# Optimization experiments

Measured on AMD Instinct MI355X. Metric: run time of the kernel, lower is better.

## Reference

```python
import jax, jax.numpy as jnp
import numpy as np

NUM_HEADS = 8


def _conv3x3(x, w, b):
    # x: (B, C, H, W); w: (O, I, 3, 3) -> (B, O, H, W), stride 1, SAME padding
    y = jax.lax.conv_general_dilated(
        x, w, window_strides=(1, 1), padding='SAME',
        dimension_numbers=('NCHW', 'OIHW', 'NCHW'))
    return y + b[None, :, None, None]


def setup_inputs() -> dict:
    key = jax.random.key(0)
    ks = jax.random.split(key, 7)
    bs, mc, C, H, W = 2, 5, 640, 32, 32
    s = 0.02  # init scale for weights
    return {
        'x': jax.random.normal(ks[0], (bs, mc, C, H, W), jnp.float32),
        'wq': jax.random.normal(ks[1], (C, C, 3, 3), jnp.float32) * s,
        'bq': jnp.zeros((C,), jnp.float32),
        'wk': jax.random.normal(ks[2], (C, C, 3, 3), jnp.float32) * s,
        'bk': jnp.zeros((C,), jnp.float32),
        'wv': jax.random.normal(ks[3], (C, C, 3, 3), jnp.float32) * s,
        'bv': jnp.zeros((C,), jnp.float32),
        'w_proj': jax.random.normal(ks[4], (C, C), jnp.float32) * s,
        'b_proj': jnp.zeros((C,), jnp.float32),
    }


def reference(x, wq, bq, wk, bk, wv, bv, w_proj, b_proj):
    bs, mc, C, H, W = x.shape
    N = H * W
    nh = NUM_HEADS
    hd = C // nh
    scale = hd ** -0.5

    xf = x.reshape(bs * mc, C, H, W)

    def proj(w, b):
        # conv -> (bs, mc, nh, hd, N) -> (bs, mc, nh, N, hd)
        y = _conv3x3(xf, w, b).reshape(bs, mc, nh, hd, N)
        return y.transpose(0, 1, 2, 4, 3)

    q = proj(wq, bq)
    k = proj(wk, bk)
    v = proj(wv, bv)

    attn = jax.nn.softmax(jnp.einsum('bmhnd,bmhkd->bmhnk', q, k) * scale, axis=-1)
    o = jnp.einsum('bmhnk,bmhkd->bmhnd', attn, v)  # (bs, mc, nh, N, hd)

    # permute(0,3,1,2,4).reshape(bs, N, mc*C) then split back to (bs, N, mc, C)
    o = o.transpose(0, 3, 1, 2, 4).reshape(bs, N, mc, C)
    o = jnp.einsum('bnmc,dc->bnmd', o, w_proj) + b_proj  # Linear(C, C)
    return o.reshape(bs, N, mc * C)
```

## Files before the change

### kernel.cpp

```cpp
#include <hip/hip_runtime.h>

typedef _Float16 half_t;
typedef _Float16 half8 __attribute__((ext_vector_type(8)));
typedef _Float16 half4 __attribute__((ext_vector_type(4)));
typedef float floatx4 __attribute__((ext_vector_type(4)));
typedef unsigned int u32;

#define MFMA32(a,b,c) __builtin_amdgcn_mfma_f32_16x16x32_f16(a,b,c,0,0,0)
#define MFMA16(a,b,c) __builtin_amdgcn_mfma_f32_16x16x16f16(a,b,c,0,0,0)

#define XPAD_ELEMS (10u*34*34*640)
#define WR_ELEMS   (3u*9*640*640)
#define WP_ELEMS   (640u*640)
#define QKV_ELEMS  (10u*8*1024*80)
#define O_ELEMS    (10u*1024*640)

__device__ __forceinline__ void load16_lds(half_t* lds, const half_t* g) {
  __builtin_amdgcn_global_load_lds((const __attribute__((address_space(1))) u32*)g,
                                   (__attribute__((address_space(3))) u32*)lds,
                                   16, 0, 0);
}

__global__ __launch_bounds__(256) void k_convert_x(const float* __restrict__ x,
                                                   half_t* __restrict__ xpad) {
  const int img = blockIdx.x >> 5, y = blockIdx.x & 31;
  const float* src = x + (size_t)img*640*1024 + y*32;
  half_t* dst = xpad + (size_t)img*34*34*640;
  for (int i = threadIdx.x; i < 640*32; i += 256) {
    int xx = i / 640, c = i - xx*640;
    float v = src[(size_t)c*1024 + xx];
    dst[((size_t)(y+1)*34 + xx + 1)*640 + c] = (half_t)v;
  }
}

__global__ __launch_bounds__(256) void k_convert_w(const float* __restrict__ wq,
                                                   const float* __restrict__ wk,
                                                   const float* __restrict__ wv,
                                                   const float* __restrict__ wp,
                                                   half_t* __restrict__ wr2,
                                                   half_t* __restrict__ wp16) {
  const int p = blockIdx.y, row = blockIdx.x;
  if (p < 3) {
    const float* W = (p == 0) ? wq : (p == 1) ? wk : wv;
    for (int i = threadIdx.x; i < 5760; i += 256) {
      int t = i / 640, ci = i - t*640;
      wr2[(((size_t)p*640 + row)*9 + t)*640 + ci] = (half_t)W[((size_t)row*640 + ci)*9 + t];
    }
  } else {
    for (int i = threadIdx.x; i < 640; i += 256)
      wp16[(size_t)row*640 + i] = (half_t)wp[(size_t)row*640 + i];
  }
}

__global__ __launch_bounds__(256) void k_conv(const half_t* __restrict__ xpad,
                                              const half_t* __restrict__ wr2,
                                              const float* __restrict__ bq,
                                              const float* __restrict__ bk,
                                              const float* __restrict__ bv,
                                              half_t* __restrict__ qo,
                                              half_t* __restrict__ ko,
                                              half_t* __restrict__ vo) {
  __shared__ __align__(16) half_t sX[2][816*8];
  __shared__ __align__(16) half_t sW[4][512*8];
  const int tid = threadIdx.x;
  const int lane = tid & 63, wv = tid >> 6;
  const int l15 = lane & 15, lq = lane >> 4, lq16 = lq*16;
  const int mt = blockIdx.x, nt = blockIdx.y;
  const int proj = blockIdx.z / 10, img = blockIdx.z - proj*10;

  const half_t* xg = xpad + ((size_t)img*34*34 + (size_t)mt*4*34)*640;
  const half_t* wg = wr2 + ((size_t)proj*640 + nt*128)*5760;

  int xsrc[4], wsrc[2];
#pragma unroll
  for (int kk = 0; kk < 4; ++kk) {
    int idx = kk*256 + tid;
    int row = idx >> 2, slot = idx & 3;
    int chunk = slot ^ ((row >> 1) & 3);
    xsrc[kk] = row*640 + chunk*8;
  }
#pragma unroll
  for (int kk = 0; kk < 2; ++kk) {
    int idx = kk*256 + tid;
    int row = idx >> 2, slot = idx & 3;
    int chunk = slot ^ ((row >> 1) & 3);
    wsrc[kk] = row*5760 + chunk*8;
  }

  const int wrow = (wv >> 1)*64, wcol = (wv & 1)*64;
  int arow0[4];
#pragma unroll
  for (int fr = 0; fr < 4; ++fr) {
    int p = wrow + fr*16 + l15;
    arow0[fr] = (p >> 5)*34 + (p & 31);
  }
  int bboff[4];
#pragma unroll
  for (int fc = 0; fc < 4; ++fc) {
    int r = wcol + fc*16 + l15;
    bboff[fc] = (r << 6) + (lq16 ^ (((r >> 1) & 3) << 4));
  }

#pragma unroll
  for (int kk = 0; kk < 4; ++kk)
    if (kk < 3 || tid < 48)
      load16_lds(sX[0] + (size_t)(kk*256 + wv*64)*8, xg + xsrc[kk]);
#pragma unroll
  for (int kk = 0; kk < 2; ++kk)
    load16_lds(sW[0] + (size_t)(kk*256 + wv*64)*8, wg + wsrc[kk]);
#pragma unroll
  for (int kk = 0; kk < 2; ++kk)
    load16_lds(sW[1] + (size_t)(kk*256 + wv*64)*8, wg + wsrc[kk] + 640);

  floatx4 acc[4][4] = {};

  for (int g = 0; g < 20; ++g) {
#pragma unroll
    for (int t = 0; t < 9; ++t) {
      if (!(g == 19 && t >= 7)) {
        const int t2 = (t + 2 < 9) ? t + 2 : t - 7;
        const int g2 = (t + 2 < 9) ? g : g + 1;
        const int k0 = t2*640 + g2*32;
        half_t* wd = sW[(g + t + 2) & 3];
#pragma unroll
        for (int kk = 0; kk < 2; ++kk)
          load16_lds(wd + (size_t)(kk*256 + wv*64)*8, wg + wsrc[kk] + k0);
      }
      if (t == 7 && g < 19) {
        half_t* xd = sX[(g + 1) & 1];
#pragma unroll
        for (int kk = 0; kk < 4; ++kk)
          if (kk < 3 || tid < 48)
            load16_lds(xd + (size_t)(kk*256 + wv*64)*8, xg + xsrc[kk] + (g + 1)*32);
      }
      if (g == 19 && t == 7)      asm volatile("s_waitcnt vmcnt(2)" ::: "memory");
      else if (g == 19 && t == 8) asm volatile("s_waitcnt vmcnt(0)" ::: "memory");
      else if (t >= 7)            asm volatile("s_waitcnt vmcnt(8)" ::: "memory");
      else                        asm volatile("s_waitcnt vmcnt(4)" ::: "memory");
      __builtin_amdgcn_s_barrier();
      __builtin_amdgcn_sched_barrier(0);
      const char* sXc = (const char*)sX[g & 1];
      const char* sWc = (const char*)sW[(g + t) & 3];
      const int TR = (t/3)*34 + (t - (t/3)*3);
      half8 av[4], bw[4];
#pragma unroll
      for (int fr = 0; fr < 4; ++fr) {
        int r = arow0[fr] + TR;
        av[fr] = *(const half8*)(sXc + (r << 6) + (lq16 ^ (((r >> 1) & 3) << 4)));
      }
#pragma unroll
      for (int fc = 0; fc < 4; ++fc) bw[fc] = *(const half8*)(sWc + bboff[fc]);
      __builtin_amdgcn_s_setprio(1);
#pragma unroll
      for (int fr = 0; fr < 4; ++fr)
#pragma unroll
        for (int fc = 0; fc < 4; ++fc)
          acc[fr][fc] = MFMA32(av[fr], bw[fc], acc[fr][fc]);
      __builtin_amdgcn_s_setprio(0);
    }
  }

  const float* bias = (proj == 0) ? bq : (proj == 1) ? bk : bv;
#pragma unroll
  for (int fc = 0; fc < 4; ++fc) {
    int co = nt*128 + wcol + fc*16 + l15;
    float bb = bias[co];
    int hh = co / 80;
    int d = co - hh*80;
#pragma unroll
    for (int fr = 0; fr < 4; ++fr)
#pragma unroll
      for (int j = 0; j < 4; ++j) {
        int n = mt*128 + wrow + fr*16 + lq*4 + j;
        float val = acc[fr][fc][j] + bb;
        if (proj == 0)      qo[((size_t)(img*8 + hh)*1024 + n)*80 + d] = (half_t)(val * 0.11180339887498949f);
        else if (proj == 1) ko[((size_t)(img*8 + hh)*1024 + n)*80 + d] = (half_t)val;
        else                vo[((size_t)(img*8 + hh)*80 + d)*1024 + n] = (half_t)val;
      }
  }
}

__global__ __launch_bounds__(256) void k_attn(const half_t* __restrict__ qg_,
                                              const half_t* __restrict__ kg_,
                                              const half_t* __restrict__ vg_,
                                              half_t* __restrict__ og_) {
  __shared__ __align__(16) half_t sQ[128*80];
  __shared__ __align__(16) half_t sK[64*80];
  __shared__ __align__(16) half_t sV[80*64];
  __shared__ __align__(16) half_t sP[128*64];
  const int tid = threadIdx.x, lane = tid & 63, wv = tid >> 6;
  const int l15 = lane & 15, lq = lane >> 4;
  const int qt = blockIdx.x, gh = blockIdx.y;
  const half_t* qg = qg_ + ((size_t)gh*1024 + qt*128)*80;
  const half_t* kg = kg_ + (size_t)gh*1024*80;
  const half_t* vg = vg_ + (size_t)gh*80*1024;

#pragma unroll
  for (int kk = 0; kk < 5; ++kk)
    load16_lds(sQ + (size_t)(kk*256 + wv*64)*8, qg + (size_t)(kk*256 + tid)*8);

  float mrow[2][4], lrow[2][4];
  floatx4 oacc[2][5] = {};
#pragma unroll
  for (int fr = 0; fr < 2; ++fr)
#pragma unroll
    for (int j = 0; j < 4; ++j) { mrow[fr][j] = -1e30f; lrow[fr][j] = 0.f; }

  for (int kt = 0; kt < 16; ++kt) {
    __syncthreads();
#pragma unroll
    for (int kk = 0; kk < 3; ++kk) {
      int c = kk*256 + tid;
      if (c < 640) {
        int row = c / 10, cw = c - row*10;
        load16_lds(sK + (size_t)(kk*256 + wv*64)*8,
                   kg + ((size_t)kt*64 + row)*80 + cw*8);
      }
    }
#pragma unroll
    for (int kk = 0; kk < 3; ++kk) {
      int c = kk*256 + tid;
      if (c < 640) {
        load16_lds(sV + (size_t)(kk*256 + wv*64)*8,
                   vg + (size_t)(c >> 3)*1024 + kt*64 + (c & 7)*8);
      }
    }
    __syncthreads();

    const char* sQb = (const char*)sQ;
    const char* sKb = (const char*)sK;
    half8 qa0[2], qa1[2]; half4 qa2[2];
#pragma unroll
    for (int fr = 0; fr < 2; ++fr) {
      int r = wv*32 + fr*16 + l15;
      qa0[fr] = *(const half8*)(sQb + r*160 + lq*16);
      qa1[fr] = *(const half8*)(sQb + r*160 + 64 + lq*16);
      qa2[fr] = *(const half4*)(sQb + r*160 + 128 + lq*8);
    }
    floatx4 s[2][4];
#pragma unroll
    for (int fc = 0; fc < 4; ++fc) {
      int key = fc*16 + l15;
      half8 kb0 = *(const half8*)(sKb + key*160 + lq*16);
      half8 kb1 = *(const half8*)(sKb + key*160 + 64 + lq*16);
      half4 kb2 = *(const half4*)(sKb + key*160 + 128 + lq*8);
#pragma unroll
      for (int fr = 0; fr < 2; ++fr) {
        floatx4 t = {0.f, 0.f, 0.f, 0.f};
        t = MFMA16(qa2[fr], kb2, t);
        t = MFMA32(qa0[fr], kb0, t);
        t = MFMA32(qa1[fr], kb1, t);
        s[fr][fc] = t;
      }
    }

    float corr[2][4], psum[2][4];
#pragma unroll
    for (int fr = 0; fr < 2; ++fr)
#pragma unroll
      for (int j = 0; j < 4; ++j) {
        float mx = fmaxf(fmaxf(s[fr][0][j], s[fr][1][j]), fmaxf(s[fr][2][j], s[fr][3][j]));
        mx = fmaxf(mx, __shfl_xor(mx, 1));
        mx = fmaxf(mx, __shfl_xor(mx, 2));
        mx = fmaxf(mx, __shfl_xor(mx, 4));
        mx = fmaxf(mx, __shfl_xor(mx, 8));
        float mn = fmaxf(mrow[fr][j], mx);
        corr[fr][j] = __expf(mrow[fr][j] - mn);
        mrow[fr][j] = mn;
        psum[fr][j] = 0.f;
      }
#pragma unroll
    for (int fc = 0; fc < 4; ++fc)
#pragma unroll
      for (int fr = 0; fr < 2; ++fr)
#pragma unroll
        for (int j = 0; j < 4; ++j) {
          float p = __expf(s[fr][fc][j] - mrow[fr][j]);
          psum[fr][j] += p;
          sP[(size_t)(wv*32 + fr*16 + lq*4 + j)*64 + fc*16 + l15] = (half_t)p;
        }
#pragma unroll
    for (int fr = 0; fr < 2; ++fr)
#pragma unroll
      for (int j = 0; j < 4; ++j) {
        float t2 = psum[fr][j];
        t2 += __shfl_xor(t2, 1);
        t2 += __shfl_xor(t2, 2);
        t2 += __shfl_xor(t2, 4);
        t2 += __shfl_xor(t2, 8);
        lrow[fr][j] = lrow[fr][j]*corr[fr][j] + t2;
      }
#pragma unroll
    for (int fr = 0; fr < 2; ++fr)
#pragma unroll
      for (int fc = 0; fc < 5; ++fc)
#pragma unroll
        for (int j = 0; j < 4; ++j)
          oacc[fr][fc][j] *= corr[fr][j];

    __syncthreads();

    const char* sPb = (const char*)sP;
    const char* sVb = (const char*)sV;
    half8 pa[2][2];
#pragma unroll
    for (int fr = 0; fr < 2; ++fr) {
      int r = wv*32 + fr*16 + l15;
#pragma unroll
      for (int ks = 0; ks < 2; ++ks)
        pa[fr][ks] = *(const half8*)(sPb + r*128 + ks*64 + lq*16);
    }
#pragma unroll
    for (int fc = 0; fc < 5; ++fc)
#pragma unroll
      for (int ks = 0; ks < 2; ++ks) {
        half8 vb = *(const half8*)(sVb + (fc*16 + l15)*128 + ks*64 + lq*16);
#pragma unroll
        for (int fr = 0; fr < 2; ++fr)
          oacc[fr][fc] = MFMA32(pa[fr][ks], vb, oacc[fr][fc]);
      }
  }

  const int img = gh >> 3, hh = gh & 7;
  half_t* og = og_ + ((size_t)img*1024 + qt*128)*640 + hh*80;
#pragma unroll
  for (int fr = 0; fr < 2; ++fr)
#pragma unroll
    for (int j = 0; j < 4; ++j) {
      int n = wv*32 + fr*16 + lq*4 + j;
      float inv = 1.f / lrow[fr][j];
#pragma unroll
      for (int fc = 0; fc < 5; ++fc)
        og[(size_t)n*640 + fc*16 + l15] = (half_t)(oacc[fr][fc][j] * inv);
    }
}

__global__ __launch_bounds__(256) void k_proj(const half_t* __restrict__ oa,
                                              const half_t* __restrict__ wp,
                                              const float* __restrict__ bp,
                                              float* __restrict__ out) {
  __shared__ __align__(16) half_t sA[128*32];
  __shared__ __align__(16) half_t sB[128*32];
  const int tid = threadIdx.x, lane = tid & 63, wv = tid >> 6;
  const int l15 = lane & 15, lq = lane >> 4;
  const int mt = blockIdx.x, nt = blockIdx.y, img = blockIdx.z;
  const int bb = img / 5, mm = img - bb*5;
  const half_t* ag = oa + ((size_t)img*1024 + mt*128)*640;
  const half_t* bg = wp + (size_t)nt*128*640;
  const int wrow = (wv >> 1)*64, wcol = (wv & 1)*64;
  floatx4 acc[4][4] = {};
  for (int g = 0; g < 20; ++g) {
    __syncthreads();
#pragma unroll
    for (int kk = 0; kk < 2; ++kk) {
      int c = kk*256 + tid;
      load16_lds(sA + (size_t)(kk*256 + wv*64)*8, ag + (size_t)(c >> 2)*640 + g*32 + (c & 3)*8);
      load16_lds(sB + (size_t)(kk*256 + wv*64)*8, bg + (size_t)(c >> 2)*640 + g*32 + (c & 3)*8);
    }
    __syncthreads();
    const char* sAb = (const char*)sA;
    const char* sBb = (const char*)sB;
    half8 av[4], bw[4];
#pragma unroll
    for (int fr = 0; fr < 4; ++fr) av[fr] = *(const half8*)(sAb + (wrow + fr*16 + l15)*64 + lq*16);
#pragma unroll
    for (int fc = 0; fc < 4; ++fc) bw[fc] = *(const half8*)(sBb + (wcol + fc*16 + l15)*64 + lq*16);
#pragma unroll
    for (int fr = 0; fr < 4; ++fr)
#pragma unroll
      for (int fc = 0; fc < 4; ++fc)
        acc[fr][fc] = MFMA32(av[fr], bw[fc], acc[fr][fc]);
  }
  float* og = out + ((size_t)bb*1024 + mt*128)*3200 + mm*640 + nt*128;
#pragma unroll
  for (int fc = 0; fc < 4; ++fc) {
    float bias = bp[nt*128 + wcol + fc*16 + l15];
#pragma unroll
    for (int fr = 0; fr < 4; ++fr)
#pragma unroll
      for (int j = 0; j < 4; ++j)
        og[(size_t)(wrow + fr*16 + lq*4 + j)*3200 + wcol + fc*16 + l15] = acc[fr][fc][j] + bias;
  }
}

extern "C" void kernel_launch(void* const* d_in, const int* in_sizes, int n_in,
                              void* d_out, int out_size, void* d_ws, size_t ws_size,
                              hipStream_t stream) {
  const float* x  = (const float*)d_in[0];
  const float* wq = (const float*)d_in[1];
  const float* bq = (const float*)d_in[2];
  const float* wk = (const float*)d_in[3];
  const float* bk = (const float*)d_in[4];
  const float* wv = (const float*)d_in[5];
  const float* bv = (const float*)d_in[6];
  const float* wp = (const float*)d_in[7];
  const float* bp = (const float*)d_in[8];
  float* out = (float*)d_out;

  half_t* xpad = (half_t*)d_ws;
  half_t* wr2  = xpad + XPAD_ELEMS;
  half_t* wp16 = wr2 + WR_ELEMS;
  half_t* q    = wp16 + WP_ELEMS;
  half_t* k    = q + QKV_ELEMS;
  half_t* v    = k + QKV_ELEMS;
  half_t* oa   = v + QKV_ELEMS;

  (void)hipMemsetAsync(xpad, 0, (size_t)XPAD_ELEMS*sizeof(half_t), stream);
  k_convert_x<<<320, 256, 0, stream>>>(x, xpad);
  k_convert_w<<<dim3(640, 4), 256, 0, stream>>>(wq, wk, wv, wp, wr2, wp16);
  k_conv<<<dim3(8, 5, 30), 256, 0, stream>>>(xpad, wr2, bq, bk, bv, q, k, v);
  k_attn<<<dim3(8, 80), 256, 0, stream>>>(q, k, v, oa);
  k_proj<<<dim3(8, 5, 10), 256, 0, stream>>>(oa, wp16, bp, out);
}
```

Baseline: 455.0 us.

## Software-pipeline conv K-loop with register double-buffered fragments and deeper weight prefetch

Restructures the implicit-GEMM conv main loop so the LDS fragments for the next step are read into a second register set while the MFMAs for the current step run, using ping-pong register buffers across an unrolled two-group loop. It also deepens the weight-tile prefetch from two steps ahead to three, and moves the input tile prefetch earlier. The goal is to hide LDS read latency and global-to-LDS load latency behind MFMA work. The cost is higher register pressure, with waitcnt values chosen per wave that must match the exact load counts to stay correct.

```diff
diff --git a/kernel.cpp b/kernel.cpp
--- a/kernel.cpp
+++ b/kernel.cpp
@@ -106,59 +106,98 @@
     if (kk < 3 || tid < 48)
       load16_lds(sX[0] + (size_t)(kk*256 + wv*64)*8, xg + xsrc[kk]);
 #pragma unroll
-  for (int kk = 0; kk < 2; ++kk)
-    load16_lds(sW[0] + (size_t)(kk*256 + wv*64)*8, wg + wsrc[kk]);
-#pragma unroll
-  for (int kk = 0; kk < 2; ++kk)
-    load16_lds(sW[1] + (size_t)(kk*256 + wv*64)*8, wg + wsrc[kk] + 640);
+  for (int st = 0; st < 3; ++st) {
+    load16_lds(sW[st] + (size_t)(wv*64)*8,       wg + wsrc[0] + st*640);
+    load16_lds(sW[st] + (size_t)(256 + wv*64)*8, wg + wsrc[1] + st*640);
+  }
+  asm volatile("s_waitcnt vmcnt(0)" ::: "memory");
+  __builtin_amdgcn_s_barrier();
 
   floatx4 acc[4][4] = {};
-
-  for (int g = 0; g < 20; ++g) {
-#pragma unroll
-    for (int t = 0; t < 9; ++t) {
-      if (!(g == 19 && t >= 7)) {
-        const int t2 = (t + 2 < 9) ? t + 2 : t - 7;
-        const int g2 = (t + 2 < 9) ? g : g + 1;
-        const int k0 = t2*640 + g2*32;
-        half_t* wd = sW[(g + t + 2) & 3];
-#pragma unroll
-        for (int kk = 0; kk < 2; ++kk)
-          load16_lds(wd + (size_t)(kk*256 + wv*64)*8, wg + wsrc[kk] + k0);
-      }
-      if (t == 7 && g < 19) {
-        half_t* xd = sX[(g + 1) & 1];
-#pragma unroll
-        for (int kk = 0; kk < 4; ++kk)
-          if (kk < 3 || tid < 48)
-            load16_lds(xd + (size_t)(kk*256 + wv*64)*8, xg + xsrc[kk] + (g + 1)*32);
-      }
-      if (g == 19 && t == 7)      asm volatile("s_waitcnt vmcnt(2)" ::: "memory");
-      else if (g == 19 && t == 8) asm volatile("s_waitcnt vmcnt(0)" ::: "memory");
-      else if (t >= 7)            asm volatile("s_waitcnt vmcnt(8)" ::: "memory");
-      else                        asm volatile("s_waitcnt vmcnt(4)" ::: "memory");
-      __builtin_amdgcn_s_barrier();
-      __builtin_amdgcn_sched_barrier(0);
-      const char* sXc = (const char*)sX[g & 1];
-      const char* sWc = (const char*)sW[(g + t) & 3];
-      const int TR = (t/3)*34 + (t - (t/3)*3);
-      half8 av[4], bw[4];
-#pragma unroll
-      for (int fr = 0; fr < 4; ++fr) {
-        int r = arow0[fr] + TR;
-        av[fr] = *(const half8*)(sXc + (r << 6) + (lq16 ^ (((r >> 1) & 3) << 4)));
-      }
-#pragma unroll
-      for (int fc = 0; fc < 4; ++fc) bw[fc] = *(const half8*)(sWc + bboff[fc]);
-      __builtin_amdgcn_s_setprio(1);
-#pragma unroll
-      for (int fr = 0; fr < 4; ++fr)
-#pragma unroll
-        for (int fc = 0; fc < 4; ++fc)
-          acc[fr][fc] = MFMA32(av[fr], bw[fc], acc[fr][fc]);
-      __builtin_amdgcn_s_setprio(0);
-    }
-  }
+  half8 Av[4], Aw[4], Bv[4], Bw[4];
+
+  {
+    const char* sXc = (const char*)sX[0];
+    const char* sWc = (const char*)sW[0];
+#pragma unroll
+    for (int fr = 0; fr < 4; ++fr) {
+      int r = arow0[fr];
+      Av[fr] = *(const half8*)(sXc + (r << 6) + (lq16 ^ (((r >> 1) & 3) << 4)));
+    }
+#pragma unroll
+    for (int fc = 0; fc < 4; ++fc) Aw[fc] = *(const half8*)(sWc + bboff[fc]);
+  }
+
+#define STEP(T, g, CURv, CURw, NXTv, NXTw) do {                                    \
+    const int s_ = 9*(g) + (T);                                                    \
+    if (s_ + 3 <= 179) {                                                           \
+      const int t3 = ((T) + 3) % 9;                                                \
+      const int g3 = (g) + ((T) + 3) / 9;                                          \
+      const int k0 = t3*640 + g3*32;                                               \
+      half_t* wd = sW[(s_ + 3) & 3];                                               \
+      load16_lds(wd + (size_t)(wv*64)*8,       wg + wsrc[0] + k0);                 \
+      load16_lds(wd + (size_t)(256 + wv*64)*8, wg + wsrc[1] + k0);                 \
+    }                                                                              \
+    if ((T) == 5 && (g) < 19) {                                                    \
+      half_t* xd = sX[((g) + 1) & 1];                                              \
+      _Pragma("unroll")                                                            \
+      for (int kk = 0; kk < 4; ++kk)                                               \
+        if (kk < 3 || tid < 48)                                                    \
+          load16_lds(xd + (size_t)(kk*256 + wv*64)*8, xg + xsrc[kk] + ((g)+1)*32); \
+    }                                                                              \
+    if ((T) >= 5 && (T) <= 7 && (g) < 19) {                                        \
+      if (wv == 0) asm volatile("s_waitcnt vmcnt(8)" ::: "memory");                \
+      else         asm volatile("s_waitcnt vmcnt(7)" ::: "memory");                \
+    } else if (s_ <= 176) asm volatile("s_waitcnt vmcnt(4)" ::: "memory");         \
+    else if (s_ == 177)   asm volatile("s_waitcnt vmcnt(2)" ::: "memory");         \
+    else                  asm volatile("s_waitcnt vmcnt(0)" ::: "memory");         \
+    __builtin_amdgcn_s_barrier();                                                  \
+    __builtin_amdgcn_sched_barrier(0);                                             \
+    if (s_ < 179) {                                                                \
+      const int tn = ((T) + 1) % 9;                                                \
+      const int gn = (g) + ((T) + 1) / 9;                                          \
+      const int TRn = (tn/3)*34 + (tn - (tn/3)*3);                                 \
+      const char* sXc = (const char*)sX[gn & 1];                                   \
+      const char* sWc = (const char*)sW[(s_ + 1) & 3];                             \
+      _Pragma("unroll")                                                            \
+      for (int fr = 0; fr < 4; ++fr) {                                             \
+        int r = arow0[fr] + TRn;                                                   \
+        NXTv[fr] = *(const half8*)(sXc + (r << 6) + (lq16 ^ (((r >> 1) & 3) << 4)));\
+      }                                                                            \
+      _Pragma("unroll")                                                            \
+      for (int fc = 0; fc < 4; ++fc) NXTw[fc] = *(const half8*)(sWc + bboff[fc]);  \
+    }                                                                              \
+    __builtin_amdgcn_sched_barrier(0);                                             \
+    __builtin_amdgcn_s_setprio(1);                                                 \
+    _Pragma("unroll")                                                              \
+    for (int fr = 0; fr < 4; ++fr)                                                 \
+      _Pragma("unroll")                                                            \
+      for (int fc = 0; fc < 4; ++fc)                                               \
+        acc[fr][fc] = MFMA32(CURv[fr], CURw[fc], acc[fr][fc]);                     \
+    __builtin_amdgcn_s_setprio(0);                                                 \
+  } while (0)
+
+  for (int gg = 0; gg < 20; gg += 2) {
+    STEP(0, gg, Av, Aw, Bv, Bw);
+    STEP(1, gg, Bv, Bw, Av, Aw);
+    STEP(2, gg, Av, Aw, Bv, Bw);
+    STEP(3, gg, Bv, Bw, Av, Aw);
+    STEP(4, gg, Av, Aw, Bv, Bw);
+    STEP(5, gg, Bv, Bw, Av, Aw);
+    STEP(6, gg, Av, Aw, Bv, Bw);
+    STEP(7, gg, Bv, Bw, Av, Aw);
+    STEP(8, gg, Av, Aw, Bv, Bw);
+    STEP(0, gg+1, Bv, Bw, Av, Aw);
+    STEP(1, gg+1, Av, Aw, Bv, Bw);
+    STEP(2, gg+1, Bv, Bw, Av, Aw);
+    STEP(3, gg+1, Av, Aw, Bv, Bw);
+    STEP(4, gg+1, Bv, Bw, Av, Aw);
+    STEP(5, gg+1, Av, Aw, Bv, Bw);
+    STEP(6, gg+1, Bv, Bw, Av, Aw);
+    STEP(7, gg+1, Av, Aw, Bv, Bw);
+    STEP(8, gg+1, Bv, Bw, Av, Aw);
+  }
+#undef STEP
 
   const float* bias = (proj == 0) ? bq : (proj == 1) ? bk : bv;
 #pragma unroll
```

Result: no change. 454.5 us (-0.1%).
